# Kernel optimization log

Hardware: AMD Instinct MI355X
Metric: run time of the kernel (lower is better)

The kernel has to match this reference:

```python
import jax, jax.numpy as jnp
import numpy as np

T, S, B = 8192, 1024, 8192


def setup_inputs() -> dict:
    key = jax.random.key(0)
    k1, k2, k3, k4, k5, k6 = jax.random.split(key, 6)
    return {
        "t": jax.random.randint(k1, (B,), 0, T),
        "s": jax.random.randint(k2, (B,), 0, S),
        "obs": jax.random.randint(k3, (T, S), 0, 5).astype(jnp.int32),
        "alpha": jax.random.uniform(k4, (S, S), dtype=jnp.float32),
        "beta": jax.random.uniform(k5, (1,), jnp.float32, 0.1, 1.0),
        "mu": jax.random.uniform(k6, (S,), dtype=jnp.float32),
    }


def reference(t, s, obs, alpha, beta, mu):
    # lam(t,s) = relu( mu[s] + beta * sum_{tp<t, sp} alpha[sp,s]*obs[tp,sp]*exp(-beta*(t-tp)) )
    # Exact rewrite of the O(T^2*S) brute force:
    #   c[tp, s] = sum_sp obs[tp, sp] * alpha[sp, s]          (GEMM)
    #   H[t, s]  = sum_{tp<t} c[tp, s] * exp(-beta*(t-tp))    (linear recurrence)
    obs_f = obs.astype(alpha.dtype)
    c = obs_f @ alpha                      # [T, S]
    a = jnp.exp(-beta[0])                  # per-step decay

    def step(h, c_t):
        h = a * (h + c_t)                  # H[t] = a*(H[t-1] + c[t-1])
        return h, h

    _, H_tail = jax.lax.scan(step, jnp.zeros_like(c[0]), c[:-1])  # H[1..T-1]
    H = jnp.concatenate([jnp.zeros_like(c[:1]), H_tail], axis=0)  # [T, S], H[0]=0

    lam_grid = jax.nn.relu(mu[None, :] + beta[0] * H)  # [T, S]
    return lam_grid[t, s]                  # [B]
```

## Files before the change

### kernel.cpp

```cpp
#include <hip/hip_runtime.h>
#include <hip/hip_bf16.h>
#include <stdint.h>

#define T_DIM 8192
#define S_DIM 1024
#define B_DIM 8192
#define CHUNK 32
#define NCHUNK 256
#define QCAP 2048
#define PASS_ROWS 8
#define NPASS 4

#define WS_NEEDED 4194304u

__global__ void transpose_alpha_kernel(const float* __restrict__ alpha,
                                       float* __restrict__ alphaT) {
    __shared__ float tile[32][33];
    int bx = blockIdx.x * 32;
    int by = blockIdx.y * 32;
    int tx = threadIdx.x, ty = threadIdx.y;
    #pragma unroll
    for (int j = 0; j < 32; j += 8)
        tile[ty + j][tx] = alpha[(size_t)(by + ty + j) * S_DIM + bx + tx];
    __syncthreads();
    #pragma unroll
    for (int j = 0; j < 32; j += 8)
        alphaT[(size_t)(bx + ty + j) * S_DIM + by + tx] = tile[tx][ty + j];
}

__global__ __launch_bounds__(1024, 1) void hawkes_kernel(
        const int* __restrict__ tq, const int* __restrict__ sq,
        const int* __restrict__ obs,
        const float* __restrict__ beta, const float* __restrict__ mu,
        const float* __restrict__ alphaT,
        float* __restrict__ out) {
    const int k    = blockIdx.x;
    const int tid  = threadIdx.x;
    const int wv   = tid >> 6, lane = tid & 63;
    const float b  = beta[0];
    const float a  = expf(-b);
    const int  t0  = k << 5;

    __shared__ int   qtmp[QCAP];
    __shared__ int   qcnt_s;
    __shared__ float Gall[PASS_ROWS][S_DIM];

    if (tid == 0) qcnt_s = 0;
    __syncthreads();

    for (int i = tid; i < B_DIM; i += 1024) {
        int tv = tq[i];
        if ((tv >> 5) == k) {
            int p = atomicAdd(&qcnt_s, 1);
            if (p < QCAP) qtmp[p] = ((tv - t0) << 13) | i;
        }
    }

    int Dmax = ((int)(26.0f / b) + 4 + 3) & ~3;
    const int n  = t0 < Dmax ? t0 : Dmax;
    const int ts = t0 - n;
    const int Q4 = n >> 2;

    const int m  = tid >> 8;
    const int c4 = (tid & 255) << 2;
    float A4 = a * a; A4 = A4 * A4;
    float F0 = 0.f, F1 = 0.f, F2 = 0.f, F3 = 0.f;
    const int* obase = obs + (size_t)(ts + m) * S_DIM + c4;

    int q = 0;
    for (; q + 8 <= Q4; q += 8) {
        int4 o[8];
        #pragma unroll
        for (int r = 0; r < 8; ++r)
            o[r] = *(const int4*)(obase + (size_t)(q + r) * 4 * S_DIM);
        #pragma unroll
        for (int r = 0; r < 8; ++r) {
            F0 = A4 * (F0 + (float)o[r].x);
            F1 = A4 * (F1 + (float)o[r].y);
            F2 = A4 * (F2 + (float)o[r].z);
            F3 = A4 * (F3 + (float)o[r].w);
        }
    }
    for (; q < Q4; ++q) {
        int4 ov = *(const int4*)(obase + (size_t)q * 4 * S_DIM);
        F0 = A4 * (F0 + (float)ov.x);
        F1 = A4 * (F1 + (float)ov.y);
        F2 = A4 * (F2 + (float)ov.z);
        F3 = A4 * (F3 + (float)ov.w);
    }
    float inva = 1.f / a;
    float am = (m == 0) ? 1.f : (m == 1) ? inva
             : (m == 2) ? inva * inva : inva * inva * inva;
    float4 cw; cw.x = F0 * am; cw.y = F1 * am; cw.z = F2 * am; cw.w = F3 * am;
    __syncthreads();
    *(float4*)&Gall[m][c4] = cw;
    __syncthreads();
    float U = Gall[0][tid] + Gall[1][tid] + Gall[2][tid] + Gall[3][tid];
    __syncthreads();
    const int Q = qcnt_s < QCAP ? qcnt_s : QCAP;

    float G = U;
    for (int pass = 0; pass < NPASS; ++pass) {
        const int jlo = pass * PASS_ROWS;
        int o[PASS_ROWS];
        #pragma unroll
        for (int r = 0; r < PASS_ROWS; ++r)
            o[r] = obs[(size_t)(t0 + jlo + r) * S_DIM + tid];
        #pragma unroll
        for (int r = 0; r < PASS_ROWS; ++r) {
            Gall[r][tid] = G;
            G = a * (G + (float)o[r]);
        }
        __syncthreads();
        for (int p = wv; p < Q; p += 16) {
            int key = qtmp[p];
            int j = key >> 13;
            if (j < jlo || j >= jlo + PASS_ROWS) continue;
            int i = key & 8191;
            int s = sq[i];
            const float* ar = alphaT + (size_t)s * S_DIM;
            const float* gr = &Gall[j - jlo][0];
            float acc = 0.f;
            #pragma unroll
            for (int cc = 0; cc < 4; ++cc) {
                float4 gv = *(const float4*)(gr + 256 * cc + lane * 4);
                float4 av = *(const float4*)(ar + 256 * cc + lane * 4);
                acc += gv.x * av.x + gv.y * av.y + gv.z * av.z + gv.w * av.w;
            }
            #pragma unroll
            for (int off = 32; off > 0; off >>= 1)
                acc += __shfl_down(acc, off);
            if (lane == 0) {
                float lam = mu[s] + b * acc;
                out[i] = lam > 0.f ? lam : 0.f;
            }
        }
        __syncthreads();
    }
}

__global__ __launch_bounds__(1024) void chunk_all_kernel(
        const int* __restrict__ tq, const int* __restrict__ sq,
        const int* __restrict__ obs, const float* __restrict__ alpha,
        const float* __restrict__ beta, const float* __restrict__ mu,
        float* __restrict__ out) {
    const int k   = blockIdx.x;
    const int tid = threadIdx.x;
    const float b = beta[0];
    const float a = expf(-b);
    const int t0 = k << 6;
    __shared__ int   qkey[2048];
    __shared__ int   qcnt_s;
    __shared__ float wred[16];
    if (tid == 0) qcnt_s = 0;
    __syncthreads();
    for (int i = tid; i < B_DIM; i += 1024) {
        int tv = tq[i];
        if ((tv >> 6) == k) {
            int p = atomicAdd(&qcnt_s, 1);
            if (p < 2048) qkey[p] = ((tv - t0) << 13) | i;
        }
    }
    __syncthreads();
    int Q = qcnt_s; if (Q > 2048) Q = 2048;
    float G = 0.f;
    for (int tp = 0; tp < t0; tp += 8) {
        int o[8];
        #pragma unroll
        for (int r = 0; r < 8; ++r) o[r] = obs[(size_t)(tp + r) * S_DIM + tid];
        #pragma unroll
        for (int r = 0; r < 8; ++r) G = a * (G + (float)o[r]);
    }
    for (int j = 0; j < 64; ++j) {
        for (int q = 0; q < Q; ++q) {
            int key = qkey[q];
            if ((key >> 13) == j) {
                int i = key & 8191;
                int s = sq[i];
                float p = G * alpha[(size_t)tid * S_DIM + s];
                #pragma unroll
                for (int off = 32; off > 0; off >>= 1) p += __shfl_down(p, off);
                if ((tid & 63) == 0) wred[tid >> 6] = p;
                __syncthreads();
                if (tid < 64) {
                    float v = (tid < 16) ? wred[tid] : 0.f;
                    v += __shfl_down(v, 8); v += __shfl_down(v, 4);
                    v += __shfl_down(v, 2); v += __shfl_down(v, 1);
                    if (tid == 0) {
                        float lam = mu[s] + b * v;
                        out[i] = lam > 0.f ? lam : 0.f;
                    }
                }
                __syncthreads();
            }
        }
        int o = obs[(size_t)(t0 + j) * S_DIM + tid];
        G = a * (G + (float)o);
    }
}

extern "C" void kernel_launch(void* const* d_in, const int* in_sizes, int n_in,
                              void* d_out, int out_size, void* d_ws, size_t ws_size,
                              hipStream_t stream) {
    const int*   t     = (const int*)d_in[0];
    const int*   s     = (const int*)d_in[1];
    const int*   obs   = (const int*)d_in[2];
    const float* alpha = (const float*)d_in[3];
    const float* beta  = (const float*)d_in[4];
    const float* mu    = (const float*)d_in[5];
    float* out = (float*)d_out;

    if (ws_size < (size_t)WS_NEEDED || d_ws == nullptr) {
        chunk_all_kernel<<<128, 1024, 0, stream>>>(t, s, obs, alpha, beta, mu, out);
        return;
    }

    float* alphaT = (float*)d_ws;
    transpose_alpha_kernel<<<dim3(32, 32), dim3(32, 8), 0, stream>>>(alpha, alphaT);
    hawkes_kernel<<<NCHUNK, 1024, 0, stream>>>(t, s, obs, beta, mu, alphaT, out);
}
```

Baseline: 114.9 us.

## Pack obs to uint8 in a pre-pass and double the time chunk per block

A new pre-pass kernel packs the int32 observation matrix into a uint8 workspace copy. The main kernel then reads bytes for both the decay-window warm-up and the in-chunk recurrence, cutting the bytes it streams. The chunk per block also grows from 32 to 64 timesteps, which halves the block count to 128 and doubles the passes per block. The cost is an extra full read of obs every call, and only half the CUs get a block. The packing silently assumes obs values fit in 8 bits.

```diff
diff --git a/kernel.cpp b/kernel.cpp
--- a/kernel.cpp
+++ b/kernel.cpp
@@ -5,13 +5,29 @@
 #define T_DIM 8192
 #define S_DIM 1024
 #define B_DIM 8192
-#define CHUNK 32
-#define NCHUNK 256
+#define CHUNK 64
+#define NCHUNK 128
 #define QCAP 2048
 #define PASS_ROWS 8
-#define NPASS 4
-
-#define WS_NEEDED 4194304u
+#define NPASS 8
+
+#define OFF_ALPHAT 0u
+#define OFF_OBS8   4194304u
+#define WS_NEEDED  12582912u
+
+__global__ void pack_obs_kernel(const int* __restrict__ obs,
+                                unsigned char* __restrict__ obs8) {
+    int i = (blockIdx.x * 256 + threadIdx.x) * 16;
+    uint32_t w[4];
+    #pragma unroll
+    for (int g = 0; g < 4; ++g) {
+        int4 v = *(const int4*)(obs + i + g * 4);
+        w[g] = (uint32_t)v.x | ((uint32_t)v.y << 8)
+             | ((uint32_t)v.z << 16) | ((uint32_t)v.w << 24);
+    }
+    uint4 o; o.x = w[0]; o.y = w[1]; o.z = w[2]; o.w = w[3];
+    *(uint4*)(obs8 + i) = o;
+}
 
 __global__ void transpose_alpha_kernel(const float* __restrict__ alpha,
                                        float* __restrict__ alphaT) {
@@ -30,7 +46,7 @@
 
 __global__ __launch_bounds__(1024, 1) void hawkes_kernel(
         const int* __restrict__ tq, const int* __restrict__ sq,
-        const int* __restrict__ obs,
+        const unsigned char* __restrict__ obs8,
         const float* __restrict__ beta, const float* __restrict__ mu,
         const float* __restrict__ alphaT,
         float* __restrict__ out) {
@@ -39,7 +55,7 @@
     const int wv   = tid >> 6, lane = tid & 63;
     const float b  = beta[0];
     const float a  = expf(-b);
-    const int  t0  = k << 5;
+    const int  t0  = k << 6;
 
     __shared__ int   qtmp[QCAP];
     __shared__ int   qcnt_s;
@@ -50,7 +66,7 @@
 
     for (int i = tid; i < B_DIM; i += 1024) {
         int tv = tq[i];
-        if ((tv >> 5) == k) {
+        if ((tv >> 6) == k) {
             int p = atomicAdd(&qcnt_s, 1);
             if (p < QCAP) qtmp[p] = ((tv - t0) << 13) | i;
         }
@@ -65,28 +81,28 @@
     const int c4 = (tid & 255) << 2;
     float A4 = a * a; A4 = A4 * A4;
     float F0 = 0.f, F1 = 0.f, F2 = 0.f, F3 = 0.f;
-    const int* obase = obs + (size_t)(ts + m) * S_DIM + c4;
+    const unsigned char* obase = obs8 + (size_t)(ts + m) * S_DIM + c4;
 
     int q = 0;
     for (; q + 8 <= Q4; q += 8) {
-        int4 o[8];
+        uint32_t o[8];
         #pragma unroll
         for (int r = 0; r < 8; ++r)
-            o[r] = *(const int4*)(obase + (size_t)(q + r) * 4 * S_DIM);
+            o[r] = *(const uint32_t*)(obase + (size_t)(q + r) * 4 * S_DIM);
         #pragma unroll
         for (int r = 0; r < 8; ++r) {
-            F0 = A4 * (F0 + (float)o[r].x);
-            F1 = A4 * (F1 + (float)o[r].y);
-            F2 = A4 * (F2 + (float)o[r].z);
-            F3 = A4 * (F3 + (float)o[r].w);
+            F0 = A4 * (F0 + (float)( o[r]        & 0xFF));
+            F1 = A4 * (F1 + (float)((o[r] >>  8) & 0xFF));
+            F2 = A4 * (F2 + (float)((o[r] >> 16) & 0xFF));
+            F3 = A4 * (F3 + (float)( o[r] >> 24));
         }
     }
     for (; q < Q4; ++q) {
-        int4 ov = *(const int4*)(obase + (size_t)q * 4 * S_DIM);
-        F0 = A4 * (F0 + (float)ov.x);
-        F1 = A4 * (F1 + (float)ov.y);
-        F2 = A4 * (F2 + (float)ov.z);
-        F3 = A4 * (F3 + (float)ov.w);
+        uint32_t ov = *(const uint32_t*)(obase + (size_t)q * 4 * S_DIM);
+        F0 = A4 * (F0 + (float)( ov        & 0xFF));
+        F1 = A4 * (F1 + (float)((ov >>  8) & 0xFF));
+        F2 = A4 * (F2 + (float)((ov >> 16) & 0xFF));
+        F3 = A4 * (F3 + (float)( ov >> 24));
     }
     float inva = 1.f / a;
     float am = (m == 0) ? 1.f : (m == 1) ? inva
@@ -102,10 +118,10 @@
     float G = U;
     for (int pass = 0; pass < NPASS; ++pass) {
         const int jlo = pass * PASS_ROWS;
-        int o[PASS_ROWS];
+        unsigned char o[PASS_ROWS];
         #pragma unroll
         for (int r = 0; r < PASS_ROWS; ++r)
-            o[r] = obs[(size_t)(t0 + jlo + r) * S_DIM + tid];
+            o[r] = obs8[(size_t)(t0 + jlo + r) * S_DIM + tid];
         #pragma unroll
         for (int r = 0; r < PASS_ROWS; ++r) {
             Gall[r][tid] = G;
@@ -215,7 +231,11 @@
         return;
     }
 
-    float* alphaT = (float*)d_ws;
+    char* ws = (char*)d_ws;
+    float*         alphaT = (float*)(ws + OFF_ALPHAT);
+    unsigned char* obs8   = (unsigned char*)(ws + OFF_OBS8);
+
+    pack_obs_kernel<<<T_DIM * S_DIM / (256 * 16), 256, 0, stream>>>(obs, obs8);
     transpose_alpha_kernel<<<dim3(32, 32), dim3(32, 8), 0, stream>>>(alpha, alphaT);
-    hawkes_kernel<<<NCHUNK, 1024, 0, stream>>>(t, s, obs, beta, mu, alphaT, out);
-}
+    hawkes_kernel<<<NCHUNK, 1024, 0, stream>>>(t, s, obs8, beta, mu, alphaT, out);
+}
```

Result: slower. 120.0 us (+4.4%).
